# Performance work log

Hardware: AMD Instinct MI355X
Metric: run time of the kernel (lower is better)

The kernel has to match this reference:

```python
import jax, jax.numpy as jnp
import numpy as np

N_NODES = 50000
N_EDGES = 800000
D = 128


def setup_inputs() -> dict:
    key = jax.random.key(0)
    ks = jax.random.split(key, 7)
    return {
        "shape_features": jax.random.normal(ks[0], (N_NODES, D), dtype=jnp.float32),
        "W1": jax.random.normal(ks[1], (D, D), dtype=jnp.float32) * 0.05,
        "b1": jax.random.normal(ks[2], (D,), dtype=jnp.float32) * 0.05,
        "W2": jax.random.normal(ks[3], (D, D), dtype=jnp.float32) * 0.05,
        "b2": jax.random.normal(ks[4], (D,), dtype=jnp.float32) * 0.05,
        "edge_src": jax.random.randint(ks[5], (N_EDGES,), 0, N_NODES, dtype=jnp.int32),
        "edge_dst": jax.random.randint(ks[6], (N_EDGES,), 0, N_NODES, dtype=jnp.int32),
    }


def reference(shape_features, W1, b1, W2, b2, edge_src, edge_dst):
    # out1 = linear1(x)  (torch Linear: x @ W.T + b)
    out1 = jnp.einsum("nd,od->no", shape_features, W1) + b1
    # ragged neighbour gather + sum per destination node (segment reduce)
    aggr = jax.ops.segment_sum(shape_features[edge_src], edge_dst,
                               num_segments=shape_features.shape[0])
    # out = linear1(x) + linear2(aggr)
    return out1 + jnp.einsum("nd,od->no", aggr, W2) + b2
```

## Files before the change

kernel.cpp:

```cpp
#include <hip/hip_runtime.h>
#include <hip/hip_bf16.h>

#define DF 128
#define BSH 5
#define BNODES 32
#define NBMAX 1600
#define CHUNK 2048
#define BMAX 400
#define TILE 2048
#define ASTRIDE 64
#define SRCMASK 0x07ffffffu

typedef __attribute__((ext_vector_type(8))) short short8;
typedef __attribute__((ext_vector_type(4))) float floatx4;

__device__ __forceinline__ ushort f2bf(float f) {
    __hip_bfloat16 h = __float2bfloat16(f);
    return *reinterpret_cast<ushort*>(&h);
}

__global__ __launch_bounds__(256) void prep_kernel(
    const float* __restrict__ x, ushort* __restrict__ xbf, int n4,
    const float* __restrict__ W1, const float* __restrict__ W2,
    const float* __restrict__ b1, const float* __restrict__ b2,
    ushort* __restrict__ w1bf, ushort* __restrict__ w2bf, float* __restrict__ bias,
    const int* __restrict__ dst, int* __restrict__ histG,
    int n_edges, int B_, int nb)
{
    __shared__ int h[NBMAX];
    int bid = blockIdx.x;
    if (bid < B_) {
        for (int j = threadIdx.x; j < nb; j += 256) h[j] = 0;
        __syncthreads();
        int base = bid * CHUNK;
#pragma unroll
        for (int i = 0; i < CHUNK / 256; ++i) {
            int e = base + i * 256 + threadIdx.x;
            if (e < n_edges) atomicAdd(&h[dst[e] >> BSH], 1);
        }
        __syncthreads();
        for (int j = threadIdx.x; j < nb; j += 256)
            histG[bid * nb + j] = h[j];
    } else if (bid < B_ + 64) {
        int i = (bid - B_) * 256 + threadIdx.x;
        if (i < DF * DF) {
            w1bf[i] = f2bf(W1[i]);
            w2bf[i] = f2bf(W2[i]);
        }
        if (i < DF) bias[i] = b1[i] + b2[i];
    } else {
        int i = (bid - B_ - 64) * 256 + threadIdx.x;
        if (i < n4) {
            float4 v = reinterpret_cast<const float4*>(x)[i];
            ushort4 o;
            o.x = f2bf(v.x); o.y = f2bf(v.y); o.z = f2bf(v.z); o.w = f2bf(v.w);
            reinterpret_cast<ushort4*>(xbf)[i] = o;
        }
    }
}

__global__ __launch_bounds__(256) void scan_local_kernel(
    const int* __restrict__ cnt, int* __restrict__ offs,
    int* __restrict__ bsum, int n)
{
    __shared__ int sd[256];
    int t = threadIdx.x;
    int base = blockIdx.x * 1024 + t * 4;

    int4 v = make_int4(0, 0, 0, 0);
    if (base + 3 < n) {
        v = *reinterpret_cast<const int4*>(cnt + base);
    } else {
        if (base + 0 < n) v.x = cnt[base + 0];
        if (base + 1 < n) v.y = cnt[base + 1];
        if (base + 2 < n) v.z = cnt[base + 2];
        if (base + 3 < n) v.w = cnt[base + 3];
    }
    int s = v.x + v.y + v.z + v.w;
    sd[t] = s;
    __syncthreads();
    for (int off = 1; off < 256; off <<= 1) {
        int u = (t >= off) ? sd[t - off] : 0;
        __syncthreads();
        sd[t] += u;
        __syncthreads();
    }
    int incl = sd[t];
    int excl = incl - s;
    if (t == 255) bsum[blockIdx.x] = incl;

    int p0 = excl, p1 = p0 + v.x, p2 = p1 + v.y, p3 = p2 + v.z;
    if (base + 0 < n) offs[base + 0] = p0;
    if (base + 1 < n) offs[base + 1] = p1;
    if (base + 2 < n) offs[base + 2] = p2;
    if (base + 3 < n) offs[base + 3] = p3;
}

__global__ __launch_bounds__(1024) void scan_bsum_kernel(
    int* __restrict__ bsum, int nb2)
{
    __shared__ int sd[1024];
    int t = threadIdx.x;
    int v = (t < nb2) ? bsum[t] : 0;
    sd[t] = v;
    __syncthreads();
    for (int off = 1; off < 1024; off <<= 1) {
        int u = (t >= off) ? sd[t - off] : 0;
        __syncthreads();
        sd[t] += u;
        __syncthreads();
    }
    if (t < nb2) bsum[t] = sd[t] - v;
}

__global__ __launch_bounds__(256) void bin_kernel(
    const int* __restrict__ src, const int* __restrict__ dst,
    const int* __restrict__ histS, const int* __restrict__ bsum,
    uint* __restrict__ pairs, int n_edges, int B_, int nb)
{
    __shared__ int  cur[NBMAX];
    __shared__ uint stage[CHUNK];
    int blk = blockIdx.x;
    for (int j = threadIdx.x; j < nb; j += 256) {
        int idx = blk * nb + j;
        cur[j] = histS[idx] + bsum[idx >> 10];
    }
    __syncthreads();
    int base = blk * CHUNK;
    int cnt = n_edges - base; if (cnt > CHUNK) cnt = CHUNK;
    for (int i = threadIdx.x; i < cnt; i += 256) {
        int e = base + i;
        int d = dst[e];
        int j = d >> BSH;
        int p = atomicAdd(&cur[j], 1);
        stage[p - base] = (uint)src[e] | ((uint)(d & (BNODES - 1)) << 27);
    }
    __syncthreads();
    for (int i = threadIdx.x; i < cnt; i += 256)
        pairs[base + i] = stage[i];
}

__global__ __launch_bounds__(256, 8) void agg_gemm_kernel(
    const ushort* __restrict__ xbf, const uint* __restrict__ pairs,
    const int* __restrict__ histS, const int* __restrict__ bsum,
    const ushort* __restrict__ w1, const ushort* __restrict__ w2,
    const float* __restrict__ bias, float* __restrict__ out,
    int n_nodes, int n_edges, int B_, int nb, int flat)
{
    __shared__ uint sorted[TILE];
    __shared__ uint abuf[BNODES * ASTRIDE];
    __shared__ int  rstart[BMAX];
    __shared__ int  rexcl[BMAX + 1];
    __shared__ int hcnt[BNODES];
    __shared__ int hoff[BNODES + 1];
    __shared__ int hcur[BNODES];

    int blk  = blockIdx.x;
    int node0 = blk * BNODES;
    int wave = threadIdx.x >> 6;
    int lane = threadIdx.x & 63;

    for (int j = threadIdx.x; j < B_; j += 256) {
        int idx = j * nb + blk;
        int s = histS[idx] + bsum[idx >> 10];
        int idx2 = idx + 1;
        int e = (idx2 >= flat) ? n_edges : histS[idx2] + bsum[idx2 >> 10];
        rstart[j] = s;
        rexcl[j]  = e - s;
    }
    __syncthreads();
    if (threadIdx.x < 64) {
        int b0 = lane * 7;
        int tv[7];
        int ls = 0;
#pragma unroll
        for (int k = 0; k < 7; ++k) {
            int idx = b0 + k;
            tv[k] = (idx < B_) ? rexcl[idx] : 0;
            ls += tv[k];
        }
        int si = ls;
#pragma unroll
        for (int off = 1; off < 64; off <<= 1) {
            int u = __shfl_up(si, off);
            if (lane >= off) si += u;
        }
        int run = si - ls;
#pragma unroll
        for (int k = 0; k < 7; ++k) {
            int idx = b0 + k;
            if (idx < B_) rexcl[idx] = run;
            run += tv[k];
        }
        if (lane == 63) rexcl[B_] = run;
    }
    __syncthreads();
    int total = rexcl[B_];

    const char* xu = (const char*)xbf;
    uint lane4 = (uint)lane << 2;

    float2 acc[8];
#pragma unroll
    for (int i = 0; i < 8; ++i) acc[i] = make_float2(0.f, 0.f);

    for (int t0 = 0; t0 < total; t0 += TILE) {
        int cnt = total - t0; if (cnt > TILE) cnt = TILE;

        if (threadIdx.x < BNODES) hcnt[threadIdx.x] = 0;
        __syncthreads();

        uint pk_[TILE / 256];
#pragma unroll
        for (int k = 0; k < TILE / 256; ++k) {
            int i = threadIdx.x + k * 256;
            if (i < cnt) {
                int t = t0 + i;
                int lo = 0, hi = B_;
                while (lo + 1 < hi) {
                    int mid = (lo + hi) >> 1;
                    if (rexcl[mid] <= t) lo = mid; else hi = mid;
                }
                uint pk = pairs[rstart[lo] + (t - rexcl[lo])];
                pk_[k] = pk;
                atomicAdd(&hcnt[pk >> 27], 1);
            }
        }
        __syncthreads();

        if (threadIdx.x < 64) {
            int v = (lane < BNODES) ? hcnt[lane] : 0;
#pragma unroll
            for (int off = 1; off < BNODES; off <<= 1) {
                int u = __shfl_up(v, off);
                if (lane >= off) v += u;
            }
            if (lane < BNODES) {
                hoff[lane + 1] = v;
                hcur[lane] = v - hcnt[lane];
            }
            if (lane == 0) hoff[0] = 0;
        }
        __syncthreads();

#pragma unroll
        for (int k = 0; k < TILE / 256; ++k) {
            int i = threadIdx.x + k * 256;
            if (i < cnt) {
                uint pk = pk_[k];
                int p = atomicAdd(&hcur[pk >> 27], 1);
                sorted[p] = (pk & SRCMASK) << 8;
            }
        }
        __syncthreads();

#pragma unroll
        for (int i = 0; i < 8; ++i) {
            int nl = wave * 8 + i;
            int j0 = hoff[nl], j1 = hoff[nl + 1];
            float2 a = acc[i];
            int j = j0;
            for (; j + 15 < j1; j += 16) {
                uint u[16];
#pragma unroll
                for (int k = 0; k < 16; ++k)
                    u[k] = *(const uint*)(xu + (size_t)(sorted[j + k] + lane4));
#pragma unroll
                for (int k = 0; k < 16; ++k) {
                    a.x += __uint_as_float(u[k] << 16);
                    a.y += __uint_as_float(u[k] & 0xffff0000u);
                }
            }
            for (; j + 3 < j1; j += 4) {
                uint u0 = *(const uint*)(xu + (size_t)(sorted[j + 0] + lane4));
                uint u1 = *(const uint*)(xu + (size_t)(sorted[j + 1] + lane4));
                uint u2 = *(const uint*)(xu + (size_t)(sorted[j + 2] + lane4));
                uint u3 = *(const uint*)(xu + (size_t)(sorted[j + 3] + lane4));
                a.x += __uint_as_float(u0 << 16) + __uint_as_float(u1 << 16)
                     + __uint_as_float(u2 << 16) + __uint_as_float(u3 << 16);
                a.y += __uint_as_float(u0 & 0xffff0000u) + __uint_as_float(u1 & 0xffff0000u)
                     + __uint_as_float(u2 & 0xffff0000u) + __uint_as_float(u3 & 0xffff0000u);
            }
            for (; j < j1; ++j) {
                uint u = *(const uint*)(xu + (size_t)(sorted[j] + lane4));
                a.x += __uint_as_float(u << 16);
                a.y += __uint_as_float(u & 0xffff0000u);
            }
            acc[i] = a;
        }
        __syncthreads();
    }

#pragma unroll
    for (int i = 0; i < 8; ++i) {
        int nl = wave * 8 + i;
        abuf[nl * ASTRIDE + lane] =
            (uint)f2bf(acc[i].x) | ((uint)f2bf(acc[i].y) << 16);
    }
    __syncthreads();

    int quad = lane >> 4;
    int m    = lane & 15;
    int rg   = wave >> 1;
    int half = wave & 1;
    int rowL = rg * 16 + m;
    int rowG = node0 + rowL;
    int rowC = (rowG < n_nodes) ? rowG : (n_nodes - 1);

    short8 xa[4], aa[4];
#pragma unroll
    for (int ks = 0; ks < 4; ++ks) {
        xa[ks] = *reinterpret_cast<const short8*>(xbf + (size_t)rowC * DF + ks * 32 + quad * 8);
        aa[ks] = *reinterpret_cast<const short8*>(&abuf[rowL * ASTRIDE + ks * 16 + quad * 4]);
    }

    int nbase = node0 + rg * 16;
#pragma unroll
    for (int oi = 0; oi < 4; ++oi) {
        int ot = half * 4 + oi;
        int o = ot * 16 + m;
        floatx4 c = {0.f, 0.f, 0.f, 0.f};
#pragma unroll
        for (int ks = 0; ks < 4; ++ks) {
            short8 bf1 = *reinterpret_cast<const short8*>(w1 + (size_t)o * DF + ks * 32 + quad * 8);
            short8 bf2 = *reinterpret_cast<const short8*>(w2 + (size_t)o * DF + ks * 32 + quad * 8);
            c = __builtin_amdgcn_mfma_f32_16x16x32_bf16(xa[ks], bf1, c, 0, 0, 0);
            c = __builtin_amdgcn_mfma_f32_16x16x32_bf16(aa[ks], bf2, c, 0, 0, 0);
        }
        float bv = bias[o];
#pragma unroll
        for (int r = 0; r < 4; ++r) {
            int row = nbase + quad * 4 + r;
            if (row < n_nodes) out[(size_t)row * DF + o] = c[r] + bv;
        }
    }
}

extern "C" void kernel_launch(void* const* d_in, const int* in_sizes, int n_in,
                              void* d_out, int out_size, void* d_ws, size_t ws_size,
                              hipStream_t stream) {
    const float* x  = (const float*)d_in[0];
    const float* W1 = (const float*)d_in[1];
    const float* b1 = (const float*)d_in[2];
    const float* W2 = (const float*)d_in[3];
    const float* b2 = (const float*)d_in[4];
    const int* esrc = (const int*)d_in[5];
    const int* edst = (const int*)d_in[6];
    float* out = (float*)d_out;

    int n_nodes = in_sizes[0] / DF;
    int n_edges = in_sizes[5];

    int nb = (n_nodes + BNODES - 1) >> BSH;
    int B_ = (n_edges + CHUNK - 1) / CHUNK;
    int flat = nb * B_;

    auto rnd16 = [](size_t v) { return (v + 15) & ~(size_t)15; };

    char* ws = (char*)d_ws;
    ushort* xbf   = (ushort*)ws;                 ws += rnd16((size_t)n_nodes * DF * 2);
    ushort* w1bf  = (ushort*)ws;                 ws += rnd16((size_t)DF * DF * 2);
    ushort* w2bf  = (ushort*)ws;                 ws += rnd16((size_t)DF * DF * 2);
    float*  bias  = (float*)ws;                  ws += rnd16((size_t)DF * 4);
    int*    histG = (int*)ws;                    ws += rnd16((size_t)flat * 4);
    int*    histS = (int*)ws;                    ws += rnd16((size_t)(flat + 1) * 4);
    int*    bsum  = (int*)ws;                    ws += 1024 * 4;
    uint*   pairs = (uint*)ws;

    int n4 = n_nodes * DF / 4;
    int prep_blocks = B_ + 64 + (n4 + 255) / 256;
    prep_kernel<<<prep_blocks, 256, 0, stream>>>(
        x, xbf, n4, W1, W2, b1, b2, w1bf, w2bf, bias,
        edst, histG, n_edges, B_, nb);

    int nb2 = (flat + 1023) / 1024;
    scan_local_kernel<<<nb2, 256, 0, stream>>>(histG, histS, bsum, flat);
    scan_bsum_kernel<<<1, 1024, 0, stream>>>(bsum, nb2);

    bin_kernel<<<B_, 256, 0, stream>>>(esrc, edst, histS, bsum, pairs, n_edges, B_, nb);

    agg_gemm_kernel<<<nb, 256, 0, stream>>>(
        xbf, pairs, histS, bsum, w1bf, w2bf, bias, out,
        n_nodes, n_edges, B_, nb, flat);
}
```

Baseline: 165.7 us.

## Fuse histogram, scan and binning into prep kernel with per-chunk local offsets

```diff
diff --git a/kernel.cpp b/kernel.cpp
--- a/kernel.cpp
+++ b/kernel.cpp
@@ -24,32 +24,82 @@
     const float* __restrict__ W1, const float* __restrict__ W2,
     const float* __restrict__ b1, const float* __restrict__ b2,
     ushort* __restrict__ w1bf, ushort* __restrict__ w2bf, float* __restrict__ bias,
-    const int* __restrict__ dst, int* __restrict__ histG,
+    const int* __restrict__ src, const int* __restrict__ dst,
+    int* __restrict__ rowoffs, uint* __restrict__ pairs,
     int n_edges, int B_, int nb)
 {
-    __shared__ int h[NBMAX];
+    __shared__ int  h[NBMAX];
+    __shared__ int  sd[256];
+    __shared__ uint stage[CHUNK];
     int bid = blockIdx.x;
+    int tid = threadIdx.x;
+
     if (bid < B_) {
-        for (int j = threadIdx.x; j < nb; j += 256) h[j] = 0;
-        __syncthreads();
         int base = bid * CHUNK;
-#pragma unroll
-        for (int i = 0; i < CHUNK / 256; ++i) {
-            int e = base + i * 256 + threadIdx.x;
-            if (e < n_edges) atomicAdd(&h[dst[e] >> BSH], 1);
-        }
-        __syncthreads();
-        for (int j = threadIdx.x; j < nb; j += 256)
-            histG[bid * nb + j] = h[j];
+        int cnt = n_edges - base; if (cnt > CHUNK) cnt = CHUNK;
+
+        for (int j = tid; j < nb; j += 256) h[j] = 0;
+        __syncthreads();
+
+        int d[CHUNK / 256], s[CHUNK / 256];
+#pragma unroll
+        for (int k = 0; k < CHUNK / 256; ++k) {
+            int i = k * 256 + tid;
+            bool ok = i < cnt;
+            d[k] = ok ? dst[base + i] : -1;
+            s[k] = ok ? src[base + i] : 0;
+            if (ok) atomicAdd(&h[d[k] >> BSH], 1);
+        }
+        __syncthreads();
+
+        int b0 = tid * 7;
+        int tv[7];
+        int ls = 0;
+#pragma unroll
+        for (int k = 0; k < 7; ++k) {
+            int idx = b0 + k;
+            tv[k] = (idx < nb) ? h[idx] : 0;
+            ls += tv[k];
+        }
+        sd[tid] = ls;
+        __syncthreads();
+        for (int off = 1; off < 256; off <<= 1) {
+            int u = (tid >= off) ? sd[tid - off] : 0;
+            __syncthreads();
+            sd[tid] += u;
+            __syncthreads();
+        }
+        int run = sd[tid] - ls;
+
+        int* ro = rowoffs + (size_t)bid * (nb + 1);
+#pragma unroll
+        for (int k = 0; k < 7; ++k) {
+            int idx = b0 + k;
+            if (idx < nb) h[idx] = run;
+            if (idx <= nb) ro[idx] = run;
+            run += tv[k];
+        }
+        __syncthreads();
+
+#pragma unroll
+        for (int k = 0; k < CHUNK / 256; ++k) {
+            if (d[k] >= 0) {
+                int p = atomicAdd(&h[d[k] >> BSH], 1);
+                stage[p] = (uint)s[k] | ((uint)(d[k] & (BNODES - 1)) << 27);
+            }
+        }
+        __syncthreads();
+        for (int i = tid; i < cnt; i += 256)
+            pairs[base + i] = stage[i];
     } else if (bid < B_ + 64) {
-        int i = (bid - B_) * 256 + threadIdx.x;
+        int i = (bid - B_) * 256 + tid;
         if (i < DF * DF) {
             w1bf[i] = f2bf(W1[i]);
             w2bf[i] = f2bf(W2[i]);
         }
         if (i < DF) bias[i] = b1[i] + b2[i];
     } else {
-        int i = (bid - B_ - 64) * 256 + threadIdx.x;
+        int i = (bid - B_ - 64) * 256 + tid;
         if (i < n4) {
             float4 v = reinterpret_cast<const float4*>(x)[i];
             ushort4 o;
@@ -59,93 +109,12 @@
     }
 }
 
-__global__ __launch_bounds__(256) void scan_local_kernel(
-    const int* __restrict__ cnt, int* __restrict__ offs,
-    int* __restrict__ bsum, int n)
-{
-    __shared__ int sd[256];
-    int t = threadIdx.x;
-    int base = blockIdx.x * 1024 + t * 4;
-
-    int4 v = make_int4(0, 0, 0, 0);
-    if (base + 3 < n) {
-        v = *reinterpret_cast<const int4*>(cnt + base);
-    } else {
-        if (base + 0 < n) v.x = cnt[base + 0];
-        if (base + 1 < n) v.y = cnt[base + 1];
-        if (base + 2 < n) v.z = cnt[base + 2];
-        if (base + 3 < n) v.w = cnt[base + 3];
-    }
-    int s = v.x + v.y + v.z + v.w;
-    sd[t] = s;
-    __syncthreads();
-    for (int off = 1; off < 256; off <<= 1) {
-        int u = (t >= off) ? sd[t - off] : 0;
-        __syncthreads();
-        sd[t] += u;
-        __syncthreads();
-    }
-    int incl = sd[t];
-    int excl = incl - s;
-    if (t == 255) bsum[blockIdx.x] = incl;
-
-    int p0 = excl, p1 = p0 + v.x, p2 = p1 + v.y, p3 = p2 + v.z;
-    if (base + 0 < n) offs[base + 0] = p0;
-    if (base + 1 < n) offs[base + 1] = p1;
-    if (base + 2 < n) offs[base + 2] = p2;
-    if (base + 3 < n) offs[base + 3] = p3;
-}
-
-__global__ __launch_bounds__(1024) void scan_bsum_kernel(
-    int* __restrict__ bsum, int nb2)
-{
-    __shared__ int sd[1024];
-    int t = threadIdx.x;
-    int v = (t < nb2) ? bsum[t] : 0;
-    sd[t] = v;
-    __syncthreads();
-    for (int off = 1; off < 1024; off <<= 1) {
-        int u = (t >= off) ? sd[t - off] : 0;
-        __syncthreads();
-        sd[t] += u;
-        __syncthreads();
-    }
-    if (t < nb2) bsum[t] = sd[t] - v;
-}
-
-__global__ __launch_bounds__(256) void bin_kernel(
-    const int* __restrict__ src, const int* __restrict__ dst,
-    const int* __restrict__ histS, const int* __restrict__ bsum,
-    uint* __restrict__ pairs, int n_edges, int B_, int nb)
-{
-    __shared__ int  cur[NBMAX];
-    __shared__ uint stage[CHUNK];
-    int blk = blockIdx.x;
-    for (int j = threadIdx.x; j < nb; j += 256) {
-        int idx = blk * nb + j;
-        cur[j] = histS[idx] + bsum[idx >> 10];
-    }
-    __syncthreads();
-    int base = blk * CHUNK;
-    int cnt = n_edges - base; if (cnt > CHUNK) cnt = CHUNK;
-    for (int i = threadIdx.x; i < cnt; i += 256) {
-        int e = base + i;
-        int d = dst[e];
-        int j = d >> BSH;
-        int p = atomicAdd(&cur[j], 1);
-        stage[p - base] = (uint)src[e] | ((uint)(d & (BNODES - 1)) << 27);
-    }
-    __syncthreads();
-    for (int i = threadIdx.x; i < cnt; i += 256)
-        pairs[base + i] = stage[i];
-}
-
 __global__ __launch_bounds__(256, 8) void agg_gemm_kernel(
     const ushort* __restrict__ xbf, const uint* __restrict__ pairs,
-    const int* __restrict__ histS, const int* __restrict__ bsum,
+    const int* __restrict__ rowoffs,
     const ushort* __restrict__ w1, const ushort* __restrict__ w2,
     const float* __restrict__ bias, float* __restrict__ out,
-    int n_nodes, int n_edges, int B_, int nb, int flat)
+    int n_nodes, int B_, int nb)
 {
     __shared__ uint sorted[TILE];
     __shared__ uint abuf[BNODES * ASTRIDE];
@@ -159,13 +128,13 @@
     int node0 = blk * BNODES;
     int wave = threadIdx.x >> 6;
     int lane = threadIdx.x & 63;
+    int NBP = nb + 1;
 
     for (int j = threadIdx.x; j < B_; j += 256) {
-        int idx = j * nb + blk;
-        int s = histS[idx] + bsum[idx >> 10];
-        int idx2 = idx + 1;
-        int e = (idx2 >= flat) ? n_edges : histS[idx2] + bsum[idx2 >> 10];
-        rstart[j] = s;
+        const int* ro = rowoffs + (size_t)j * NBP + blk;
+        int s = ro[0];
+        int e = ro[1];
+        rstart[j] = j * CHUNK + s;
         rexcl[j]  = e - s;
     }
     __syncthreads();
@@ -353,33 +322,23 @@
 
     int nb = (n_nodes + BNODES - 1) >> BSH;
     int B_ = (n_edges + CHUNK - 1) / CHUNK;
-    int flat = nb * B_;
 
     auto rnd16 = [](size_t v) { return (v + 15) & ~(size_t)15; };
 
     char* ws = (char*)d_ws;
-    ushort* xbf   = (ushort*)ws;                 ws += rnd16((size_t)n_nodes * DF * 2);
-    ushort* w1bf  = (ushort*)ws;                 ws += rnd16((size_t)DF * DF * 2);
-    ushort* w2bf  = (ushort*)ws;                 ws += rnd16((size_t)DF * DF * 2);
-    float*  bias  = (float*)ws;                  ws += rnd16((size_t)DF * 4);
-    int*    histG = (int*)ws;                    ws += rnd16((size_t)flat * 4);
-    int*    histS = (int*)ws;                    ws += rnd16((size_t)(flat + 1) * 4);
-    int*    bsum  = (int*)ws;                    ws += 1024 * 4;
-    uint*   pairs = (uint*)ws;
+    ushort* xbf     = (ushort*)ws;               ws += rnd16((size_t)n_nodes * DF * 2);
+    ushort* w1bf    = (ushort*)ws;               ws += rnd16((size_t)DF * DF * 2);
+    ushort* w2bf    = (ushort*)ws;               ws += rnd16((size_t)DF * DF * 2);
+    float*  bias    = (float*)ws;                ws += rnd16((size_t)DF * 4);
+    int*    rowoffs = (int*)ws;                  ws += rnd16((size_t)B_ * (nb + 1) * 4);
+    uint*   pairs   = (uint*)ws;
 
     int n4 = n_nodes * DF / 4;
     int prep_blocks = B_ + 64 + (n4 + 255) / 256;
     prep_kernel<<<prep_blocks, 256, 0, stream>>>(
         x, xbf, n4, W1, W2, b1, b2, w1bf, w2bf, bias,
-        edst, histG, n_edges, B_, nb);
-
-    int nb2 = (flat + 1023) / 1024;
-    scan_local_kernel<<<nb2, 256, 0, stream>>>(histG, histS, bsum, flat);
-    scan_bsum_kernel<<<1, 1024, 0, stream>>>(bsum, nb2);
-
-    bin_kernel<<<B_, 256, 0, stream>>>(esrc, edst, histS, bsum, pairs, n_edges, B_, nb);
+        esrc, edst, rowoffs, pairs, n_edges, B_, nb);
 
     agg_gemm_kernel<<<nb, 256, 0, stream>>>(
-        xbf, pairs, histS, bsum, w1bf, w2bf, bias, out,
-        n_nodes, n_edges, B_, nb, flat);
+        xbf, pairs, rowoffs, w1bf, w2bf, bias, out, n_nodes, B_, nb);
 }
```

Measured after the change: 151.8 us (median of 2 runs). 1.09x faster.
